# Performance work log

Hardware: AMD Instinct MI355X
Metric: run time of the kernel (lower is better)

The kernel has to match this reference:

```python
import jax, jax.numpy as jnp
import numpy as np

WIN = 2  # window_size
EPS = 1e-5


def _expanded_adj(adj, n, win):
    # Faithful to original __init__: last block set to adj, then the WHOLE
    # matrix overwritten with tiled identity (original code behavior), then
    # row-normalized (norm_adj assumed row normalization).
    ea = jnp.zeros((n, n * win), adj.dtype).at[:, -n:].set(adj)
    ea = jnp.tile(jnp.eye(n, dtype=adj.dtype), (1, win))  # overwrite, as in source
    return ea / jnp.clip(ea.sum(-1, keepdims=True), 1e-12)


def setup_inputs() -> dict:
    key = jax.random.key(0)
    ks = jax.random.split(key, 4)
    B, T, N, D = 32, 24, 1000, 64
    s = 1.0 / np.sqrt(D)
    return {
        "x": jax.random.normal(ks[0], (B, T, N, D), jnp.float32),
        "adj": jax.random.uniform(ks[1], (N, N), jnp.float32),
        "w1": jax.random.normal(ks[2], (D, D), jnp.float32) * s,
        "b1": jnp.zeros((D,), jnp.float32),
        "w2": jax.random.normal(ks[3], (D, D), jnp.float32) * s,
        "b2": jnp.zeros((D,), jnp.float32),
        "gamma": jnp.ones((D,), jnp.float32),
        "beta": jnp.zeros((D,), jnp.float32),
    }


def reference(x, adj, w1, b1, w2, b2, gamma, beta):
    B, T, N, D = x.shape
    ea = _expanded_adj(adj, N, WIN)
    pad = jnp.zeros((B, WIN - 1, N, D), x.dtype)
    feat = jnp.concatenate([pad, x], axis=1)
    win = jnp.stack([feat[:, i:i + T] for i in range(WIN)], axis=2)
    g = win.reshape(B, T, WIN * N, D)  # [B,T,W*N,D]
    h1 = jnp.einsum('nm,btmd->btnd', ea, g @ w1.T + b1)
    h2 = jnp.einsum('nm,btmd->btnd', ea, g @ w2.T + b2)
    out = jax.nn.relu(h1 * h2) + h1 + x  # gated activation + residuals
    mu = out.mean(-1, keepdims=True)
    var = ((out - mu) ** 2).mean(-1, keepdims=True)
    return (out - mu) * jax.lax.rsqrt(var + EPS) * gamma + beta
```

## Files before the change

### kernel.cpp

```cpp
#include <hip/hip_runtime.h>
#include <hip/hip_bf16.h>

#define TT 24
#define NN 1000
#define DD 64
#define TCH 12
#define NCH (TT / TCH)
#define NT  63

typedef short bf16x8 __attribute__((ext_vector_type(8)));
typedef float f32x4  __attribute__((ext_vector_type(4)));

__device__ __forceinline__ short f2bf(float f) {
    __hip_bfloat16 h = __float2bfloat16(f);
    return *reinterpret_cast<short*>(&h);
}

__global__ __launch_bounds__(64, 2)
void stgcn_d2b(const float* __restrict__ x,
               const float* __restrict__ w1, const float* __restrict__ b1,
               const float* __restrict__ w2, const float* __restrict__ b2,
               const float* __restrict__ gamma, const float* __restrict__ beta,
               float* __restrict__ out)
{
    const int l   = threadIdx.x & 63;
    const int lr  = l & 15;
    const int lc  = l >> 4;

    const int w  = __builtin_amdgcn_readfirstlane(blockIdx.x);
    const int nt = w % NT;
    const int tc = (w / NT) % NCH;
    const int b  = w / (NT * NCH);
    const int t0 = tc * TCH;
    const int n0 = nt * 16;

    const int rowA = min(n0 + lr, NN - 1);
    const int offQ = rowA * DD + lc * 4;

    const size_t ts = (size_t)NN * DD;
    const float* px = x   + (size_t)(b*TT + t0) * ts;
    float*       po = out + (size_t)(b*TT + t0) * ts;

    f32x4 qA0 = *(const f32x4*)(px + offQ);
    f32x4 qA1 = *(const f32x4*)(px + offQ + 16);
    f32x4 qA2 = *(const f32x4*)(px + offQ + 32);
    f32x4 qA3 = *(const f32x4*)(px + offQ + 48);
    f32x4 qB0 = *(const f32x4*)(px + ts + offQ);
    f32x4 qB1 = *(const f32x4*)(px + ts + offQ + 16);
    f32x4 qB2 = *(const f32x4*)(px + ts + offQ + 32);
    f32x4 qB3 = *(const f32x4*)(px + ts + offQ + 48);
    f32x4 qC0, qC1, qC2, qC3;

    bf16x8 XA[2], XB[2];
    if (t0 > 0) {
        const float* pm = px - ts;
        f32x4 m0 = *(const f32x4*)(pm + offQ);
        f32x4 m1 = *(const f32x4*)(pm + offQ + 16);
        f32x4 m2 = *(const f32x4*)(pm + offQ + 32);
        f32x4 m3 = *(const f32x4*)(pm + offQ + 48);
#pragma unroll
        for (int j = 0; j < 4; ++j) {
            XA[0][j]     = f2bf(m0[j]);
            XA[0][4 + j] = f2bf(m1[j]);
            XA[1][j]     = f2bf(m2[j]);
            XA[1][4 + j] = f2bf(m3[j]);
        }
    } else {
        XA[0] = 0; XA[1] = 0;
    }

    bf16x8 W1f[4][2], W2f[4][2];
#pragma unroll
    for (int nf = 0; nf < 4; ++nf) {
#pragma unroll
        for (int ks = 0; ks < 2; ++ks) {
            const float* p1 = &w1[(size_t)(lr + 16*nf) * DD + lc*4 + 32*ks];
            const float* p2 = &w2[(size_t)(lr + 16*nf) * DD + lc*4 + 32*ks];
            f32x4 u0 = *(const f32x4*)p1, u1 = *(const f32x4*)(p1 + 16);
            f32x4 v0 = *(const f32x4*)p2, v1 = *(const f32x4*)(p2 + 16);
#pragma unroll
            for (int j = 0; j < 4; ++j) {
                W1f[nf][ks][j]     = f2bf(0.5f * u0[j]);
                W1f[nf][ks][4 + j] = f2bf(0.5f * u1[j]);
                W2f[nf][ks][j]     = f2bf(0.5f * v0[j]);
                W2f[nf][ks][4 + j] = f2bf(0.5f * v1[j]);
            }
        }
    }
    f32x4 bia1[4], bia2[4], gmm[4], btt[4];
#pragma unroll
    for (int nf = 0; nf < 4; ++nf) {
        const int d0 = 16*nf + lc*4;
        bia1[nf] = *(const f32x4*)&b1[d0];
        bia2[nf] = *(const f32x4*)&b2[d0];
        gmm[nf]  = *(const f32x4*)&gamma[d0];
        btt[nf]  = *(const f32x4*)&beta[d0];
    }

    auto step = [&](int t,
                    f32x4& q0, f32x4& q1, f32x4& q2, f32x4& q3,
                    f32x4& p0, f32x4& p1, f32x4& p2, f32x4& p3,
                    bf16x8 (&Xi)[2], bf16x8 (&Xo)[2]) {
        const float* pn = px + (size_t)min(t + 2, TCH - 1) * ts;
        p0 = *(const f32x4*)(pn + offQ);
        p1 = *(const f32x4*)(pn + offQ + 16);
        p2 = *(const f32x4*)(pn + offQ + 32);
        p3 = *(const f32x4*)(pn + offQ + 48);

        f32x4 C1[4], C2[4];
#pragma unroll
        for (int nf = 0; nf < 4; ++nf) {
            C1[nf] = __builtin_amdgcn_mfma_f32_16x16x32_bf16(W1f[nf][0], Xi[0], bia1[nf], 0, 0, 0);
            C1[nf] = __builtin_amdgcn_mfma_f32_16x16x32_bf16(W1f[nf][1], Xi[1], C1[nf],   0, 0, 0);
            C2[nf] = __builtin_amdgcn_mfma_f32_16x16x32_bf16(W2f[nf][0], Xi[0], bia2[nf], 0, 0, 0);
            C2[nf] = __builtin_amdgcn_mfma_f32_16x16x32_bf16(W2f[nf][1], Xi[1], C2[nf],   0, 0, 0);
        }

#pragma unroll
        for (int j = 0; j < 4; ++j) {
            Xo[0][j]     = f2bf(q0[j]);
            Xo[0][4 + j] = f2bf(q1[j]);
            Xo[1][j]     = f2bf(q2[j]);
            Xo[1][4 + j] = f2bf(q3[j]);
        }
#pragma unroll
        for (int nf = 0; nf < 4; ++nf) {
            C1[nf] = __builtin_amdgcn_mfma_f32_16x16x32_bf16(W1f[nf][0], Xo[0], C1[nf], 0, 0, 0);
            C1[nf] = __builtin_amdgcn_mfma_f32_16x16x32_bf16(W1f[nf][1], Xo[1], C1[nf], 0, 0, 0);
            C2[nf] = __builtin_amdgcn_mfma_f32_16x16x32_bf16(W2f[nf][0], Xo[0], C2[nf], 0, 0, 0);
            C2[nf] = __builtin_amdgcn_mfma_f32_16x16x32_bf16(W2f[nf][1], Xo[1], C2[nf], 0, 0, 0);
        }

        float sa = 0.f, sb = 0.f, s2a = 0.f, s2b = 0.f;
        const f32x4* xr[4] = { &q0, &q1, &q2, &q3 };
#pragma unroll
        for (int nf = 0; nf < 4; ++nf) {
#pragma unroll
            for (int i = 0; i < 4; ++i) {
                float h1 = C1[nf][i];
                float h2 = C2[nf][i];
                float pg = h1 * h2;
                float oo = (pg > 0.f ? pg : 0.f) + h1 + (*xr[nf])[i];
                C1[nf][i] = oo;
                if (nf & 1) { sb += oo; s2b = fmaf(oo, oo, s2b); }
                else        { sa += oo; s2a = fmaf(oo, oo, s2a); }
            }
        }
        float s  = sa + sb;
        float s2 = s2a + s2b;
        s  += __shfl_xor(s,  16, 64);  s  += __shfl_xor(s,  32, 64);
        s2 += __shfl_xor(s2, 16, 64);  s2 += __shfl_xor(s2, 32, 64);
        float mu = s * (1.f/64.f);
        float va = fmaf(s2, 1.f/64.f, -mu*mu);
        float rs = rsqrtf(va + 1e-5f);

        if (n0 + lr < NN) {
            float* pot = po + (size_t)t * ts;
#pragma unroll
            for (int nf = 0; nf < 4; ++nf) {
                f32x4 v;
#pragma unroll
                for (int i = 0; i < 4; ++i)
                    v[i] = fmaf((C1[nf][i] - mu) * rs, gmm[nf][i], btt[nf][i]);
                __builtin_nontemporal_store(v, (f32x4*)(pot + offQ + 16*nf));
            }
        }
    };

#pragma unroll 1
    for (int tb = 0; tb < TCH; tb += 6) {
        step(tb + 0, qA0,qA1,qA2,qA3,  qC0,qC1,qC2,qC3,  XA, XB);
        step(tb + 1, qB0,qB1,qB2,qB3,  qA0,qA1,qA2,qA3,  XB, XA);
        step(tb + 2, qC0,qC1,qC2,qC3,  qB0,qB1,qB2,qB3,  XA, XB);
        step(tb + 3, qA0,qA1,qA2,qA3,  qC0,qC1,qC2,qC3,  XB, XA);
        step(tb + 4, qB0,qB1,qB2,qB3,  qA0,qA1,qA2,qA3,  XA, XB);
        step(tb + 5, qC0,qC1,qC2,qC3,  qB0,qB1,qB2,qB3,  XB, XA);
    }
}

extern "C" void kernel_launch(void* const* d_in, const int* in_sizes, int n_in,
                              void* d_out, int out_size, void* d_ws, size_t ws_size,
                              hipStream_t stream) {
    const float* x     = (const float*)d_in[0];
    const float* w1    = (const float*)d_in[2];
    const float* b1    = (const float*)d_in[3];
    const float* w2    = (const float*)d_in[4];
    const float* b2    = (const float*)d_in[5];
    const float* gamma = (const float*)d_in[6];
    const float* beta  = (const float*)d_in[7];
    float* out = (float*)d_out;

    dim3 grid(32 * NT * NCH);
    dim3 block(64);
    hipLaunchKernelGGL(stgcn_d2b, grid, block, 0, stream,
                       x, w1, b1, w2, b2, gamma, beta, out);
}
```

Measured before the change: 79.92 us.

## Deepen x prefetch to three timesteps and pack gamma/beta as bf16

Increases the register prefetch ring from three to four buffers so that x loads are issued three timesteps ahead instead of two, giving more memory latency hiding in this bandwidth-bound kernel. To free registers for the extra buffer, gamma and beta are stored as packed bf16 and widened at use. The cost is more VGPR pressure, which could hurt occupancy at 2 waves per SIMD, plus a small loss of precision in gamma and beta. The loop unroll changes from 6 to 4 steps to match the new ring.

```diff
diff --git a/kernel.cpp b/kernel.cpp
--- a/kernel.cpp
+++ b/kernel.cpp
@@ -9,19 +9,25 @@
 #define NT  63
 
 typedef short bf16x8 __attribute__((ext_vector_type(8)));
+typedef short bf16x4 __attribute__((ext_vector_type(4)));
 typedef float f32x4  __attribute__((ext_vector_type(4)));
 
 __device__ __forceinline__ short f2bf(float f) {
     __hip_bfloat16 h = __float2bfloat16(f);
     return *reinterpret_cast<short*>(&h);
 }
+__device__ __forceinline__ float bf2f(short s) {
+    union { unsigned u; float f; } c;
+    c.u = ((unsigned)(unsigned short)s) << 16;
+    return c.f;
+}
 
 __global__ __launch_bounds__(64, 2)
-void stgcn_d2b(const float* __restrict__ x,
-               const float* __restrict__ w1, const float* __restrict__ b1,
-               const float* __restrict__ w2, const float* __restrict__ b2,
-               const float* __restrict__ gamma, const float* __restrict__ beta,
-               float* __restrict__ out)
+void stgcn_d3(const float* __restrict__ x,
+              const float* __restrict__ w1, const float* __restrict__ b1,
+              const float* __restrict__ w2, const float* __restrict__ b2,
+              const float* __restrict__ gamma, const float* __restrict__ beta,
+              float* __restrict__ out)
 {
     const int l   = threadIdx.x & 63;
     const int lr  = l & 15;
@@ -49,7 +55,11 @@
     f32x4 qB1 = *(const f32x4*)(px + ts + offQ + 16);
     f32x4 qB2 = *(const f32x4*)(px + ts + offQ + 32);
     f32x4 qB3 = *(const f32x4*)(px + ts + offQ + 48);
-    f32x4 qC0, qC1, qC2, qC3;
+    f32x4 qC0 = *(const f32x4*)(px + 2*ts + offQ);
+    f32x4 qC1 = *(const f32x4*)(px + 2*ts + offQ + 16);
+    f32x4 qC2 = *(const f32x4*)(px + 2*ts + offQ + 32);
+    f32x4 qC3 = *(const f32x4*)(px + 2*ts + offQ + 48);
+    f32x4 qD0, qD1, qD2, qD3;
 
     bf16x8 XA[2], XB[2];
     if (t0 > 0) {
@@ -87,21 +97,24 @@
             }
         }
     }
-    f32x4 bia1[4], bia2[4], gmm[4], btt[4];
+    f32x4 bia1[4], bia2[4];
+    bf16x4 gpk[4], bpk[4];
 #pragma unroll
     for (int nf = 0; nf < 4; ++nf) {
         const int d0 = 16*nf + lc*4;
         bia1[nf] = *(const f32x4*)&b1[d0];
         bia2[nf] = *(const f32x4*)&b2[d0];
-        gmm[nf]  = *(const f32x4*)&gamma[d0];
-        btt[nf]  = *(const f32x4*)&beta[d0];
+        f32x4 g = *(const f32x4*)&gamma[d0];
+        f32x4 be = *(const f32x4*)&beta[d0];
+#pragma unroll
+        for (int i = 0; i < 4; ++i) { gpk[nf][i] = f2bf(g[i]); bpk[nf][i] = f2bf(be[i]); }
     }
 
     auto step = [&](int t,
                     f32x4& q0, f32x4& q1, f32x4& q2, f32x4& q3,
                     f32x4& p0, f32x4& p1, f32x4& p2, f32x4& p3,
                     bf16x8 (&Xi)[2], bf16x8 (&Xo)[2]) {
-        const float* pn = px + (size_t)min(t + 2, TCH - 1) * ts;
+        const float* pn = px + (size_t)min(t + 3, TCH - 1) * ts;
         p0 = *(const f32x4*)(pn + offQ);
         p1 = *(const f32x4*)(pn + offQ + 16);
         p2 = *(const f32x4*)(pn + offQ + 32);
@@ -161,20 +174,18 @@
                 f32x4 v;
 #pragma unroll
                 for (int i = 0; i < 4; ++i)
-                    v[i] = fmaf((C1[nf][i] - mu) * rs, gmm[nf][i], btt[nf][i]);
+                    v[i] = fmaf((C1[nf][i] - mu) * rs, bf2f(gpk[nf][i]), bf2f(bpk[nf][i]));
                 __builtin_nontemporal_store(v, (f32x4*)(pot + offQ + 16*nf));
             }
         }
     };
 
 #pragma unroll 1
-    for (int tb = 0; tb < TCH; tb += 6) {
-        step(tb + 0, qA0,qA1,qA2,qA3,  qC0,qC1,qC2,qC3,  XA, XB);
+    for (int tb = 0; tb < TCH; tb += 4) {
+        step(tb + 0, qA0,qA1,qA2,qA3,  qD0,qD1,qD2,qD3,  XA, XB);
         step(tb + 1, qB0,qB1,qB2,qB3,  qA0,qA1,qA2,qA3,  XB, XA);
         step(tb + 2, qC0,qC1,qC2,qC3,  qB0,qB1,qB2,qB3,  XA, XB);
-        step(tb + 3, qA0,qA1,qA2,qA3,  qC0,qC1,qC2,qC3,  XB, XA);
-        step(tb + 4, qB0,qB1,qB2,qB3,  qA0,qA1,qA2,qA3,  XA, XB);
-        step(tb + 5, qC0,qC1,qC2,qC3,  qB0,qB1,qB2,qB3,  XB, XA);
+        step(tb + 3, qD0,qD1,qD2,qD3,  qC0,qC1,qC2,qC3,  XB, XA);
     }
 }
 
@@ -192,6 +203,6 @@
 
     dim3 grid(32 * NT * NCH);
     dim3 block(64);
-    hipLaunchKernelGGL(stgcn_d2b, grid, block, 0, stream,
+    hipLaunchKernelGGL(stgcn_d3, grid, block, 0, stream,
                        x, w1, b1, w2, b2, gamma, beta, out);
 }
```

After: 89.12 us. +11.5%, slower.
